# Kernel optimization log

Hardware: AMD Instinct MI355X
Metric: run time of the kernel (lower is better)

The kernel has to match this reference:

```python
import jax, jax.numpy as jnp
import numpy as np

NUM_HEADS = 16
WINDOW = 128
PERSIST = 16


def setup_inputs() -> dict:
    key = jax.random.key(0)
    ks = jax.random.split(key, 6)
    B, S, D, L = 2, 2048, 2048, 512
    sd = 1.0 / np.sqrt(D)
    sl = 1.0 / np.sqrt(L)
    return {
        "x": jax.random.normal(ks[0], (B, S, D), dtype=jnp.float32),
        "Wq": jax.random.normal(ks[1], (D, D), dtype=jnp.float32) * sd,
        "Wkv": jax.random.normal(ks[2], (D, L), dtype=jnp.float32) * sd,
        "Wk": jax.random.normal(ks[3], (L, D), dtype=jnp.float32) * sl,
        "Wv": jax.random.normal(ks[4], (L, D), dtype=jnp.float32) * sl,
        "Wo": jax.random.normal(ks[5], (D, D), dtype=jnp.float32) * sd,
    }


def reference(x, Wq, Wkv, Wk, Wv, Wo):
    B, S, D = x.shape
    H = NUM_HEADS
    hd = D // H
    scale = hd ** -0.5

    q = (x @ Wq).reshape(B, S, H, hd)
    kv_latent = x @ Wkv                      # MLA-style latent bottleneck
    k = (kv_latent @ Wk).reshape(B, S, H, hd)
    v = (kv_latent @ Wv).reshape(B, S, H, hd)

    # causal + sliding-window + persistent attention-sink mask
    qi = jnp.arange(S)[:, None]
    ki = jnp.arange(S)[None, :]
    mask = (ki <= qi) & ((qi - ki < WINDOW) | (ki < PERSIST))  # [S,S]

    scores = jnp.einsum("bqhd,bkhd->bhqk", q, k) * scale
    scores = jnp.where(mask[None, None], scores, jnp.finfo(scores.dtype).min)
    attn = jax.nn.softmax(scores, axis=-1)
    out = jnp.einsum("bhqk,bkhd->bqhd", attn, v).reshape(B, S, D)
    return out @ Wo
```

## Files before the change

kernel.cpp:

```cpp
#include <hip/hip_runtime.h>

typedef float f32x4 __attribute__((ext_vector_type(4)));
typedef float f32x16 __attribute__((ext_vector_type(16)));
typedef __bf16 bf16x8 __attribute__((ext_vector_type(8)));
typedef short short8 __attribute__((ext_vector_type(8)));

__device__ __forceinline__ short f2bf(float f) {
    union { float f; unsigned u; } x; x.f = f;
    unsigned r = x.u + 0x7fffu + ((x.u >> 16) & 1u);
    return (short)(r >> 16);
}
__device__ __forceinline__ float bf2f(short s) {
    union { unsigned u; float f; } x;
    x.u = ((unsigned)(unsigned short)s) << 16;
    return x.f;
}

__device__ __forceinline__ void store_out(float* p, float v) { *p = v; }
__device__ __forceinline__ void store_out(short* p, float v) { *p = f2bf(v); }

__device__ __forceinline__ void gload_lds16(const short* g, short* l) {
    __builtin_amdgcn_global_load_lds(
        (__attribute__((address_space(1))) void*)(void*)g,
        (__attribute__((address_space(3))) void*)l, 16, 0, 0);
}

__global__ void prep_all(const float* __restrict__ x, short* __restrict__ xb,
                         const float* __restrict__ Wq, const float* __restrict__ Wo,
                         const float* __restrict__ Wk, const float* __restrict__ Wv,
                         const float* __restrict__ Wkv,
                         short* __restrict__ WqkvT, short* __restrict__ WoT,
                         short* __restrict__ WkT, short* __restrict__ WvT) {
    __shared__ float tile[32][33];
    int id = blockIdx.x;
    const int t = threadIdx.x;
    if (id < 8192) {
        const int i = id * 256 + t;
        float4 v = ((const float4*)x)[i];
        ((short4*)xb)[i] = make_short4(f2bf(v.x), f2bf(v.y), f2bf(v.z), f2bf(v.w));
        return;
    }
    id -= 8192;
    const float* in; short* out; int R, C, xt, yt;
    if (id < 4096)       { in = Wq;  out = WqkvT; R = 2048; C = 2048; xt = id & 63; yt = id >> 6; }
    else if (id < 8192)  { id -= 4096; in = Wo;  out = WoT;  R = 2048; C = 2048; xt = id & 63; yt = id >> 6; }
    else if (id < 9216)  { id -= 8192; in = Wk;  out = WkT;  R = 512;  C = 2048; xt = id & 63; yt = id >> 6; }
    else if (id < 10240) { id -= 9216; in = Wv;  out = WvT;  R = 512;  C = 2048; xt = id & 63; yt = id >> 6; }
    else                 { id -= 10240; in = Wkv; out = WqkvT + (size_t)2048 * 2048;
                           R = 2048; C = 512; xt = id & 15; yt = id >> 4; }
    const int c0 = xt * 32, r0 = yt * 32;
    const int tx = t & 31, ty = t >> 5;
#pragma unroll
    for (int i = 0; i < 32; i += 8)
        tile[ty + i][tx] = in[(size_t)(r0 + ty + i) * C + c0 + tx];
    __syncthreads();
#pragma unroll
    for (int i = 0; i < 32; i += 8)
        out[(size_t)(c0 + ty + i) * R + r0 + tx] = f2bf(tile[tx][ty + i]);
}

template <typename OutT>
__device__ __forceinline__ void gemm32_core(
    const short* __restrict__ A, const short* __restrict__ Bt, OutT* __restrict__ C,
    int m0, int n0, int K, int lda, int ldb, int ldc, short* sA, short* sB) {
    const int t = threadIdx.x;
    const int w = t >> 6, l = t & 63;
    const int wr = w >> 1, wc = w & 1;
    const int lrow = l & 31, lhalf = l >> 5;

    f32x16 acc[2][2] = {};

    const int r_off = w * 32 + (l >> 3);
    const int c8 = (((l & 7) ^ (l >> 3)) & 7) * 8;
    const short* aB = A + (size_t)(m0 + r_off) * lda + c8;
    const short* bB = Bt + (size_t)(n0 + r_off) * ldb + c8;
    short* sAw = sA + w * 2048;
    short* sBw = sB + w * 2048;

    for (int kk = 0; kk < K; kk += 64) {
#pragma unroll
        for (int p = 0; p < 4; ++p) {
            gload_lds16(aB + kk + (size_t)(p * 8) * lda, sAw + p * 512);
            gload_lds16(bB + kk + (size_t)(p * 8) * ldb, sBw + p * 512);
        }
        __syncthreads();
#pragma unroll
        for (int ks = 0; ks < 4; ++ks) {
            const int c = ks * 2 + lhalf;
            bf16x8 af[2], bfr[2];
#pragma unroll
            for (int mi = 0; mi < 2; ++mi) {
                const int m = wr * 64 + mi * 32 + lrow;
                af[mi] = *(const bf16x8*)&sA[m * 64 + (c ^ (m & 7)) * 8];
            }
#pragma unroll
            for (int ni = 0; ni < 2; ++ni) {
                const int n = wc * 64 + ni * 32 + lrow;
                bfr[ni] = *(const bf16x8*)&sB[n * 64 + (c ^ (n & 7)) * 8];
            }
#pragma unroll
            for (int mi = 0; mi < 2; ++mi)
#pragma unroll
                for (int ni = 0; ni < 2; ++ni)
                    acc[mi][ni] = __builtin_amdgcn_mfma_f32_32x32x16_bf16(
                        af[mi], bfr[ni], acc[mi][ni], 0, 0, 0);
        }
        __syncthreads();
    }
#pragma unroll
    for (int mi = 0; mi < 2; ++mi)
#pragma unroll
        for (int ni = 0; ni < 2; ++ni) {
            const int col = n0 + wc * 64 + ni * 32 + lrow;
#pragma unroll
            for (int r = 0; r < 16; ++r) {
                const int row = m0 + wr * 64 + mi * 32 + (r & 3) + 8 * (r >> 2) + 4 * lhalf;
                store_out(&C[(size_t)row * ldc + col], acc[mi][ni][r]);
            }
        }
}

template <typename OutT>
__global__ __launch_bounds__(256, 2)
void gemm32(const short* __restrict__ A, const short* __restrict__ Bt,
            OutT* __restrict__ C, int K, int lda, int ldb, int ldc) {
    __shared__ __align__(16) short sA[128 * 64];
    __shared__ __align__(16) short sB[128 * 64];
    gemm32_core<OutT>(A, Bt, C, blockIdx.y * 128, blockIdx.x * 128, K, lda, ldb, ldc, sA, sB);
}

__global__ __launch_bounds__(256, 2)
void gemm32_kv(const short* __restrict__ kvl, const short* __restrict__ WkT,
               short* __restrict__ kk, const short* __restrict__ WvT,
               short* __restrict__ vT) {
    __shared__ __align__(16) short sA[128 * 64];
    __shared__ __align__(16) short sB[128 * 64];
    int id = blockIdx.x;
    if (id < 512) {
        gemm32_core<short>(kvl, WkT, kk, (id >> 4) * 128, (id & 15) * 128,
                           512, 2560, 512, 2048, sA, sB);
    } else {
        id -= 512;
        gemm32_core<short>(WvT, kvl, vT, (id >> 5) * 128, (id & 31) * 128,
                           512, 512, 2560, 4096, sA, sB);
    }
}

#define A_S 2048
#define A_D 2048
#define A_M 4096
#define A_HD 128
__global__ __launch_bounds__(256)
void attn_win3(const short* __restrict__ Q, const short* __restrict__ K,
               const short* __restrict__ vT, short* __restrict__ O, int ldq) {
    const int qt = blockIdx.x, h = blockIdx.y, b = blockIdx.z;
    const int Qs = qt * 64;
    const int t = threadIdx.x, w = t >> 6, l = t & 63;
    const int qs = Qs + w * 16;
    const int lg = l >> 4, ln = l & 15;
    const float SCALE = 0.088388347648318447f;

    __shared__ __align__(16) short sK[2][512 * 8];
    __shared__ __align__(16) short sV[2][512 * 8];
    __shared__ __align__(16) short sP[4][16][40];

    const size_t bS = (size_t)b * A_S;
    const short* qrow = Q + (bS + qs + ln) * ldq + h * A_HD;
    bf16x8 qf[4];
#pragma unroll
    for (int ks = 0; ks < 4; ++ks)
        qf[ks] = *(const bf16x8*)(qrow + ks * 32 + lg * 8);

    f32x4 o[8] = {};
    float lsum[4] = {0.f, 0.f, 0.f, 0.f};

    int C_lo = (Qs - 127) >> 5; if (C_lo < 0) C_lo = 0;
    const int C_hi = (Qs + 63) >> 5;
    const bool sink = C_lo > 0;
    const int total = (C_hi - C_lo + 1) + (sink ? 1 : 0);

    const int key0 = t >> 4, dseg0s = (t & 15) ^ (key0 & 7);
    const int d0 = t >> 2, ksg0 = (t & 3) ^ ((d0 >> 1) & 3);
    const int key1 = (256 + t) >> 4, dseg1s = (t & 15) ^ (key1 & 7);
    const int d1 = (256 + t) >> 2, ksg1 = (t & 3) ^ ((d1 >> 1) & 3);
    const short* Kb = K + bS * A_D + h * A_HD;
    const short* Vb = vT + (size_t)h * A_HD * A_M + b * A_S;

#define STAGE(kb, buf)                                                          \
    do {                                                                        \
        gload_lds16(Kb + (size_t)((kb) + key0) * A_D + dseg0s * 8,              \
                    &sK[buf][(size_t)(w * 64) * 8]);                            \
        gload_lds16(Vb + (size_t)d0 * A_M + (kb) + ksg0 * 8,                    \
                    &sV[buf][(size_t)(w * 64) * 8]);                            \
        gload_lds16(Kb + (size_t)((kb) + key1) * A_D + dseg1s * 8,              \
                    &sK[buf][(size_t)(256 + w * 64) * 8]);                      \
        gload_lds16(Vb + (size_t)d1 * A_M + (kb) + ksg1 * 8,                    \
                    &sV[buf][(size_t)(256 + w * 64) * 8]);                      \
    } while (0)

#define CHUNK_KB(ci) ((((sink) && (ci) == 0) ? 0 : (C_lo + (ci) - (sink ? 1 : 0))) * 32)

    STAGE(CHUNK_KB(0), 0);
    __syncthreads();

    for (int ci = 0; ci < total; ++ci) {
        if (ci + 1 < total) {
            const int nkb = CHUNK_KB(ci + 1);
            STAGE(nkb, (ci + 1) & 1);
        }
        const int kb = CHUNK_KB(ci);
        const int buf = ci & 1;
        const bool any = (kb < 16) || ((kb + 31 >= qs - 127) && (kb <= qs + 15));
        if (any) {
            f32x4 s0 = {0.f, 0.f, 0.f, 0.f}, s1 = {0.f, 0.f, 0.f, 0.f};
#pragma unroll
            for (int ks = 0; ks < 4; ++ks) {
                const int dsg = ks * 4 + lg;
                bf16x8 k0 = *(const bf16x8*)&sK[buf][(ln * 16 + (dsg ^ (ln & 7))) * 8];
                bf16x8 k1 = *(const bf16x8*)&sK[buf][((16 + ln) * 16 + (dsg ^ (ln & 7))) * 8];
                s0 = __builtin_amdgcn_mfma_f32_16x16x32_bf16(qf[ks], k0, s0, 0, 0, 0);
                s1 = __builtin_amdgcn_mfma_f32_16x16x32_bf16(qf[ks], k1, s1, 0, 0, 0);
            }
            const int k0i = kb + ln, k1i = kb + 16 + ln;
#pragma unroll
            for (int r = 0; r < 4; ++r) {
                const int qi = qs + lg * 4 + r;
                const bool m0 = (k0i <= qi) && ((qi - k0i < 128) || (k0i < 16));
                const bool m1 = (k1i <= qi) && ((qi - k1i < 128) || (k1i < 16));
                const float p0 = m0 ? __expf(s0[r] * SCALE) : 0.f;
                const float p1 = m1 ? __expf(s1[r] * SCALE) : 0.f;
                lsum[r] += p0 + p1;
                sP[w][lg * 4 + r][ln] = f2bf(p0);
                sP[w][lg * 4 + r][16 + ln] = f2bf(p1);
            }
            bf16x8 pf = *(const bf16x8*)&sP[w][ln][lg * 8];
#pragma unroll
            for (int dgi = 0; dgi < 8; ++dgi) {
                const int d = dgi * 16 + ln;
                bf16x8 vf = *(const bf16x8*)&sV[buf][(d * 4 + (lg ^ ((ln >> 1) & 3))) * 8];
                o[dgi] = __builtin_amdgcn_mfma_f32_16x16x32_bf16(pf, vf, o[dgi], 0, 0, 0);
            }
        }
        __syncthreads();
    }
#undef STAGE
#undef CHUNK_KB

#pragma unroll
    for (int r = 0; r < 4; ++r) {
        float s = lsum[r];
        s += __shfl_xor(s, 1); s += __shfl_xor(s, 2);
        s += __shfl_xor(s, 4); s += __shfl_xor(s, 8);
        const float inv = 1.0f / s;
        short* orow = O + (bS + qs + lg * 4 + r) * A_D + h * A_HD + ln;
#pragma unroll
        for (int dgi = 0; dgi < 8; ++dgi)
            orow[dgi * 16] = f2bf(o[dgi][r] * inv);
    }
}

extern "C" void kernel_launch(void* const* d_in, const int* in_sizes, int n_in,
                              void* d_out, int out_size, void* d_ws, size_t ws_size,
                              hipStream_t stream) {
    (void)in_sizes; (void)n_in; (void)out_size; (void)ws_size;
    const float* x   = (const float*)d_in[0];
    const float* Wq  = (const float*)d_in[1];
    const float* Wkv = (const float*)d_in[2];
    const float* Wk  = (const float*)d_in[3];
    const float* Wv  = (const float*)d_in[4];
    const float* Wo  = (const float*)d_in[5];
    float* out = (float*)d_out;

    const int B = 2, S = 2048, D = 2048, L = 512, H = 16;
    const int M = B * S;
    const int NQ = D + L;

    short* p = (short*)d_ws;
    short* xb    = p; p += (size_t)M * D;
    short* WqkvT = p; p += (size_t)NQ * D;
    short* WkT   = p; p += (size_t)D * L;
    short* WvT   = p; p += (size_t)D * L;
    short* WoT   = p; p += (size_t)D * D;
    short* qkv   = p; p += (size_t)M * NQ;
    short* kk    = p; p += (size_t)M * D;
    short* vT    = p; p += (size_t)D * M;
    short* ao    = p; p += (size_t)M * D;

    prep_all<<<19456, 256, 0, stream>>>(x, xb, Wq, Wo, Wk, Wv, Wkv,
                                        WqkvT, WoT, WkT, WvT);
    gemm32<short><<<dim3(NQ / 128, M / 128), 256, 0, stream>>>(
        xb, WqkvT, qkv, D, D, D, NQ);
    gemm32_kv<<<1024, 256, 0, stream>>>(qkv + D, WkT, kk, WvT, vT);

    attn_win3<<<dim3(S / 64, H, B), 256, 0, stream>>>(qkv, kk, vT, ao, NQ);

    gemm32<float><<<dim3(D / 128, M / 128), 256, 0, stream>>>(
        ao, WoT, out, D, D, D, D);
}
```

Baseline: 272.1 us.

## Switch GEMMs to 16x16 MFMA and load attention K/V directly from global

The GEMM core now uses 16x16x32 bf16 MFMA with a 4x4 accumulator grid per wave instead of 32x32x16 with 2x2. This changes the LDS read pattern and the epilogue store layout. The attention kernel drops its shared-memory double-buffered K/V staging and barriers. Each wave now reads K and V fragments straight from global memory, iterating only over the chunks its own 16 query rows need, which removes block-wide syncs and some wasted chunks. In exchange, K/V reuse across the four waves goes through cache instead of LDS.

After: 297.9 us. +9.5%, slower.

```diff
diff --git a/kernel.cpp b/kernel.cpp
--- a/kernel.cpp
+++ b/kernel.cpp
@@ -1,7 +1,6 @@
 #include <hip/hip_runtime.h>
 
 typedef float f32x4 __attribute__((ext_vector_type(4)));
-typedef float f32x16 __attribute__((ext_vector_type(16)));
 typedef __bf16 bf16x8 __attribute__((ext_vector_type(8)));
 typedef short short8 __attribute__((ext_vector_type(8)));
 
@@ -9,11 +8,6 @@
     union { float f; unsigned u; } x; x.f = f;
     unsigned r = x.u + 0x7fffu + ((x.u >> 16) & 1u);
     return (short)(r >> 16);
-}
-__device__ __forceinline__ float bf2f(short s) {
-    union { unsigned u; float f; } x;
-    x.u = ((unsigned)(unsigned short)s) << 16;
-    return x.f;
 }
 
 __device__ __forceinline__ void store_out(float* p, float v) { *p = v; }
@@ -60,15 +54,15 @@
 }
 
 template <typename OutT>
-__device__ __forceinline__ void gemm32_core(
+__device__ __forceinline__ void gemm16_core(
     const short* __restrict__ A, const short* __restrict__ Bt, OutT* __restrict__ C,
     int m0, int n0, int K, int lda, int ldb, int ldc, short* sA, short* sB) {
     const int t = threadIdx.x;
     const int w = t >> 6, l = t & 63;
     const int wr = w >> 1, wc = w & 1;
-    const int lrow = l & 31, lhalf = l >> 5;
-
-    f32x16 acc[2][2] = {};
+    const int lg = l >> 4, ln = l & 15;
+
+    f32x4 acc[4][4] = {};
 
     const int r_off = w * 32 + (l >> 3);
     const int c8 = (((l & 7) ^ (l >> 3)) & 7) * 8;
@@ -85,63 +79,60 @@
         }
         __syncthreads();
 #pragma unroll
-        for (int ks = 0; ks < 4; ++ks) {
-            const int c = ks * 2 + lhalf;
-            bf16x8 af[2], bfr[2];
-#pragma unroll
-            for (int mi = 0; mi < 2; ++mi) {
-                const int m = wr * 64 + mi * 32 + lrow;
-                af[mi] = *(const bf16x8*)&sA[m * 64 + (c ^ (m & 7)) * 8];
-            }
-#pragma unroll
-            for (int ni = 0; ni < 2; ++ni) {
-                const int n = wc * 64 + ni * 32 + lrow;
-                bfr[ni] = *(const bf16x8*)&sB[n * 64 + (c ^ (n & 7)) * 8];
-            }
-#pragma unroll
-            for (int mi = 0; mi < 2; ++mi)
-#pragma unroll
-                for (int ni = 0; ni < 2; ++ni)
-                    acc[mi][ni] = __builtin_amdgcn_mfma_f32_32x32x16_bf16(
+        for (int ks = 0; ks < 2; ++ks) {
+            const int pos = (((ks * 4 + lg) ^ (ln & 7)) & 7) * 8;
+            bf16x8 af[4], bfr[4];
+#pragma unroll
+            for (int mi = 0; mi < 4; ++mi)
+                af[mi] = *(const bf16x8*)&sA[(wr * 64 + mi * 16 + ln) * 64 + pos];
+#pragma unroll
+            for (int ni = 0; ni < 4; ++ni)
+                bfr[ni] = *(const bf16x8*)&sB[(wc * 64 + ni * 16 + ln) * 64 + pos];
+#pragma unroll
+            for (int mi = 0; mi < 4; ++mi)
+#pragma unroll
+                for (int ni = 0; ni < 4; ++ni)
+                    acc[mi][ni] = __builtin_amdgcn_mfma_f32_16x16x32_bf16(
                         af[mi], bfr[ni], acc[mi][ni], 0, 0, 0);
         }
         __syncthreads();
     }
 #pragma unroll
-    for (int mi = 0; mi < 2; ++mi)
-#pragma unroll
-        for (int ni = 0; ni < 2; ++ni) {
-            const int col = n0 + wc * 64 + ni * 32 + lrow;
-#pragma unroll
-            for (int r = 0; r < 16; ++r) {
-                const int row = m0 + wr * 64 + mi * 32 + (r & 3) + 8 * (r >> 2) + 4 * lhalf;
+    for (int mi = 0; mi < 4; ++mi) {
+#pragma unroll
+        for (int ni = 0; ni < 4; ++ni) {
+            const int col = n0 + wc * 64 + ni * 16 + ln;
+#pragma unroll
+            for (int r = 0; r < 4; ++r) {
+                const int row = m0 + wr * 64 + mi * 16 + lg * 4 + r;
                 store_out(&C[(size_t)row * ldc + col], acc[mi][ni][r]);
             }
         }
+    }
 }
 
 template <typename OutT>
 __global__ __launch_bounds__(256, 2)
-void gemm32(const short* __restrict__ A, const short* __restrict__ Bt,
+void gemm16(const short* __restrict__ A, const short* __restrict__ Bt,
             OutT* __restrict__ C, int K, int lda, int ldb, int ldc) {
     __shared__ __align__(16) short sA[128 * 64];
     __shared__ __align__(16) short sB[128 * 64];
-    gemm32_core<OutT>(A, Bt, C, blockIdx.y * 128, blockIdx.x * 128, K, lda, ldb, ldc, sA, sB);
+    gemm16_core<OutT>(A, Bt, C, blockIdx.y * 128, blockIdx.x * 128, K, lda, ldb, ldc, sA, sB);
 }
 
 __global__ __launch_bounds__(256, 2)
-void gemm32_kv(const short* __restrict__ kvl, const short* __restrict__ WkT,
+void gemm16_kv(const short* __restrict__ kvl, const short* __restrict__ WkT,
                short* __restrict__ kk, const short* __restrict__ WvT,
                short* __restrict__ vT) {
     __shared__ __align__(16) short sA[128 * 64];
     __shared__ __align__(16) short sB[128 * 64];
     int id = blockIdx.x;
     if (id < 512) {
-        gemm32_core<short>(kvl, WkT, kk, (id >> 4) * 128, (id & 15) * 128,
+        gemm16_core<short>(kvl, WkT, kk, (id >> 4) * 128, (id & 15) * 128,
                            512, 2560, 512, 2048, sA, sB);
     } else {
         id -= 512;
-        gemm32_core<short>(WvT, kvl, vT, (id >> 5) * 128, (id & 31) * 128,
+        gemm16_core<short>(WvT, kvl, vT, (id >> 5) * 128, (id & 31) * 128,
                            512, 512, 2560, 4096, sA, sB);
     }
 }
@@ -151,17 +142,14 @@
 #define A_M 4096
 #define A_HD 128
 __global__ __launch_bounds__(256)
-void attn_win3(const short* __restrict__ Q, const short* __restrict__ K,
+void attn_win4(const short* __restrict__ Q, const short* __restrict__ K,
                const short* __restrict__ vT, short* __restrict__ O, int ldq) {
     const int qt = blockIdx.x, h = blockIdx.y, b = blockIdx.z;
-    const int Qs = qt * 64;
     const int t = threadIdx.x, w = t >> 6, l = t & 63;
-    const int qs = Qs + w * 16;
+    const int qs = qt * 64 + w * 16;
     const int lg = l >> 4, ln = l & 15;
     const float SCALE = 0.088388347648318447f;
 
-    __shared__ __align__(16) short sK[2][512 * 8];
-    __shared__ __align__(16) short sV[2][512 * 8];
     __shared__ __align__(16) short sP[4][16][40];
 
     const size_t bS = (size_t)b * A_S;
@@ -174,77 +162,46 @@
     f32x4 o[8] = {};
     float lsum[4] = {0.f, 0.f, 0.f, 0.f};
 
-    int C_lo = (Qs - 127) >> 5; if (C_lo < 0) C_lo = 0;
-    const int C_hi = (Qs + 63) >> 5;
-    const bool sink = C_lo > 0;
-    const int total = (C_hi - C_lo + 1) + (sink ? 1 : 0);
-
-    const int key0 = t >> 4, dseg0s = (t & 15) ^ (key0 & 7);
-    const int d0 = t >> 2, ksg0 = (t & 3) ^ ((d0 >> 1) & 3);
-    const int key1 = (256 + t) >> 4, dseg1s = (t & 15) ^ (key1 & 7);
-    const int d1 = (256 + t) >> 2, ksg1 = (t & 3) ^ ((d1 >> 1) & 3);
+    int clo = (qs - 127) >> 5; if (clo < 0) clo = 0;
+    const int chi = (qs + 15) >> 5;
+    const bool sink = clo > 0;
+    const int nch = (chi - clo + 1) + (sink ? 1 : 0);
+
     const short* Kb = K + bS * A_D + h * A_HD;
     const short* Vb = vT + (size_t)h * A_HD * A_M + b * A_S;
 
-#define STAGE(kb, buf)                                                          \
-    do {                                                                        \
-        gload_lds16(Kb + (size_t)((kb) + key0) * A_D + dseg0s * 8,              \
-                    &sK[buf][(size_t)(w * 64) * 8]);                            \
-        gload_lds16(Vb + (size_t)d0 * A_M + (kb) + ksg0 * 8,                    \
-                    &sV[buf][(size_t)(w * 64) * 8]);                            \
-        gload_lds16(Kb + (size_t)((kb) + key1) * A_D + dseg1s * 8,              \
-                    &sK[buf][(size_t)(256 + w * 64) * 8]);                      \
-        gload_lds16(Vb + (size_t)d1 * A_M + (kb) + ksg1 * 8,                    \
-                    &sV[buf][(size_t)(256 + w * 64) * 8]);                      \
-    } while (0)
-
-#define CHUNK_KB(ci) ((((sink) && (ci) == 0) ? 0 : (C_lo + (ci) - (sink ? 1 : 0))) * 32)
-
-    STAGE(CHUNK_KB(0), 0);
-    __syncthreads();
-
-    for (int ci = 0; ci < total; ++ci) {
-        if (ci + 1 < total) {
-            const int nkb = CHUNK_KB(ci + 1);
-            STAGE(nkb, (ci + 1) & 1);
-        }
-        const int kb = CHUNK_KB(ci);
-        const int buf = ci & 1;
-        const bool any = (kb < 16) || ((kb + 31 >= qs - 127) && (kb <= qs + 15));
-        if (any) {
-            f32x4 s0 = {0.f, 0.f, 0.f, 0.f}, s1 = {0.f, 0.f, 0.f, 0.f};
-#pragma unroll
-            for (int ks = 0; ks < 4; ++ks) {
-                const int dsg = ks * 4 + lg;
-                bf16x8 k0 = *(const bf16x8*)&sK[buf][(ln * 16 + (dsg ^ (ln & 7))) * 8];
-                bf16x8 k1 = *(const bf16x8*)&sK[buf][((16 + ln) * 16 + (dsg ^ (ln & 7))) * 8];
-                s0 = __builtin_amdgcn_mfma_f32_16x16x32_bf16(qf[ks], k0, s0, 0, 0, 0);
-                s1 = __builtin_amdgcn_mfma_f32_16x16x32_bf16(qf[ks], k1, s1, 0, 0, 0);
-            }
-            const int k0i = kb + ln, k1i = kb + 16 + ln;
-#pragma unroll
-            for (int r = 0; r < 4; ++r) {
-                const int qi = qs + lg * 4 + r;
-                const bool m0 = (k0i <= qi) && ((qi - k0i < 128) || (k0i < 16));
-                const bool m1 = (k1i <= qi) && ((qi - k1i < 128) || (k1i < 16));
-                const float p0 = m0 ? __expf(s0[r] * SCALE) : 0.f;
-                const float p1 = m1 ? __expf(s1[r] * SCALE) : 0.f;
-                lsum[r] += p0 + p1;
-                sP[w][lg * 4 + r][ln] = f2bf(p0);
-                sP[w][lg * 4 + r][16 + ln] = f2bf(p1);
-            }
-            bf16x8 pf = *(const bf16x8*)&sP[w][ln][lg * 8];
-#pragma unroll
-            for (int dgi = 0; dgi < 8; ++dgi) {
-                const int d = dgi * 16 + ln;
-                bf16x8 vf = *(const bf16x8*)&sV[buf][(d * 4 + (lg ^ ((ln >> 1) & 3))) * 8];
-                o[dgi] = __builtin_amdgcn_mfma_f32_16x16x32_bf16(pf, vf, o[dgi], 0, 0, 0);
-            }
-        }
-        __syncthreads();
-    }
-#undef STAGE
-#undef CHUNK_KB
+    for (int ci = 0; ci < nch; ++ci) {
+        const int kb = ((sink && ci == 0) ? 0 : (clo + ci - (sink ? 1 : 0))) * 32;
+        const short* krow0 = Kb + (size_t)(kb + ln) * A_D + lg * 8;
+        const short* krow1 = Kb + (size_t)(kb + 16 + ln) * A_D + lg * 8;
+        f32x4 s0 = {0.f, 0.f, 0.f, 0.f}, s1 = {0.f, 0.f, 0.f, 0.f};
+#pragma unroll
+        for (int ks = 0; ks < 4; ++ks) {
+            bf16x8 k0 = *(const bf16x8*)(krow0 + ks * 32);
+            bf16x8 k1 = *(const bf16x8*)(krow1 + ks * 32);
+            s0 = __builtin_amdgcn_mfma_f32_16x16x32_bf16(qf[ks], k0, s0, 0, 0, 0);
+            s1 = __builtin_amdgcn_mfma_f32_16x16x32_bf16(qf[ks], k1, s1, 0, 0, 0);
+        }
+        const int k0i = kb + ln, k1i = kb + 16 + ln;
+#pragma unroll
+        for (int r = 0; r < 4; ++r) {
+            const int qi = qs + lg * 4 + r;
+            const bool m0 = (k0i <= qi) && ((qi - k0i < 128) || (k0i < 16));
+            const bool m1 = (k1i <= qi) && ((qi - k1i < 128) || (k1i < 16));
+            const float p0 = m0 ? __expf(s0[r] * SCALE) : 0.f;
+            const float p1 = m1 ? __expf(s1[r] * SCALE) : 0.f;
+            lsum[r] += p0 + p1;
+            sP[w][lg * 4 + r][ln] = f2bf(p0);
+            sP[w][lg * 4 + r][16 + ln] = f2bf(p1);
+        }
+        bf16x8 pf = *(const bf16x8*)&sP[w][ln][lg * 8];
+        const short* vcol = Vb + kb + lg * 8;
+#pragma unroll
+        for (int dgi = 0; dgi < 8; ++dgi) {
+            bf16x8 vf = *(const bf16x8*)(vcol + (size_t)(dgi * 16 + ln) * A_M);
+            o[dgi] = __builtin_amdgcn_mfma_f32_16x16x32_bf16(pf, vf, o[dgi], 0, 0, 0);
+        }
+    }
 
 #pragma unroll
     for (int r = 0; r < 4; ++r) {
@@ -288,12 +245,12 @@
 
     prep_all<<<19456, 256, 0, stream>>>(x, xb, Wq, Wo, Wk, Wv, Wkv,
                                         WqkvT, WoT, WkT, WvT);
-    gemm32<short><<<dim3(NQ / 128, M / 128), 256, 0, stream>>>(
+    gemm16<short><<<dim3(NQ / 128, M / 128), 256, 0, stream>>>(
         xb, WqkvT, qkv, D, D, D, NQ);
-    gemm32_kv<<<1024, 256, 0, stream>>>(qkv + D, WkT, kk, WvT, vT);
-
-    attn_win3<<<dim3(S / 64, H, B), 256, 0, stream>>>(qkv, kk, vT, ao, NQ);
-
-    gemm32<float><<<dim3(D / 128, M / 128), 256, 0, stream>>>(
+    gemm16_kv<<<1024, 256, 0, stream>>>(qkv + D, WkT, kk, WvT, vT);
+
+    attn_win4<<<dim3(S / 64, H, B), 256, 0, stream>>>(qkv, kk, vT, ao, NQ);
+
+    gemm16<float><<<dim3(D / 128, M / 128), 256, 0, stream>>>(
         ao, WoT, out, D, D, D, D);
 }
```
